# Optimization experiments

Hardware: AMD Instinct MI355X
Metric: run time of the kernel (lower is better)

## Reference

```python
import jax, jax.numpy as jnp
import numpy as np

D = 128

def setup_inputs() -> dict:
    key = jax.random.key(0)
    k1, k2, k3, k4, k5, k6, k7 = jax.random.split(key, 7)
    B, L = 2048, 200
    target = jax.random.normal(k1, (B, D), dtype=jnp.float32)
    item_seq = jax.random.normal(k2, (B, L, D), dtype=jnp.float32)
    seq_len = jax.random.randint(k3, (B,), 0, 200, dtype=jnp.int64 if jax.config.jax_enable_x64 else jnp.int32)
    # MLP params: Linear(4D -> 2D), Linear(2D -> 1), PyTorch-style init scale
    s1 = 1.0 / np.sqrt(4 * D)
    s2 = 1.0 / np.sqrt(2 * D)
    W1 = jax.random.uniform(k4, (4 * D, 2 * D), minval=-s1, maxval=s1, dtype=jnp.float32)
    b1 = jax.random.uniform(k5, (2 * D,), minval=-s1, maxval=s1, dtype=jnp.float32)
    W2 = jax.random.uniform(k6, (2 * D, 1), minval=-s2, maxval=s2, dtype=jnp.float32)
    b2 = jax.random.uniform(k7, (1,), minval=-s2, maxval=s2, dtype=jnp.float32)
    return {"target": target, "item_seq": item_seq, "seq_len": seq_len,
            "W1": W1, "b1": b1, "W2": W2, "b2": b2}

def reference(target, item_seq, seq_len, W1, b1, W2, b2):
    B, L, Dd = item_seq.shape
    t = target[:, None, :]                              # B 1 D (broadcast over L)
    tgt = jnp.broadcast_to(t, (B, L, Dd))
    sub = item_seq - tgt
    dot = item_seq * tgt
    mlp_in = jnp.concatenate([tgt, item_seq, sub, dot], axis=-1)   # B L 4D
    h = jax.nn.relu(jnp.einsum('blf,fh->blh', mlp_in, W1) + b1)    # B L 2D
    score = jnp.einsum('blh,ho->blo', h, W2) + b2                  # B L 1
    mask = (jnp.arange(L)[None, :] < seq_len[:, None]).astype(item_seq.dtype)  # B L
    weighted = score * item_seq * mask[:, :, None]                 # B L D
    return jnp.sum(weighted, axis=1)                               # B D
```

## Files before the change

### kernel.cpp

```cpp
#include <hip/hip_runtime.h>
#include <hip/hip_bf16.h>

typedef short short8 __attribute__((ext_vector_type(8)));
typedef float f32x4 __attribute__((ext_vector_type(4)));

#define XSTRIDE 264

static __device__ inline short f2bf(float f) {
    unsigned u = __float_as_uint(f);
    unsigned r = (u + 0x7fffu + ((u >> 16) & 1u)) >> 16;
    return (short)r;
}
static __device__ inline float bf2f(short s) {
    return __uint_as_float(((unsigned)(unsigned short)s) << 16);
}

__global__ void prep(const float* __restrict__ W1, float* __restrict__ Wu,
                     short* __restrict__ Wfrag, float* __restrict__ out) {
    int idx = blockIdx.x * 256 + threadIdx.x;
    if (idx < 32768) {
        Wu[idx] = W1[idx] - W1[idx + 256 * 256];
    } else if (idx < 98304) {
        int i = idx - 32768;
        int j = i & 7;
        int l = (i >> 3) & 63;
        int s = (i >> 9) & 7;
        int t = i >> 12;
        int k = s * 32 + ((l >> 4) << 3) + j;
        int n = t * 16 + (l & 15);
        float v;
        if (k < 128) v = W1[(128 + k) * 256 + n] + W1[(256 + k) * 256 + n];
        else         v = W1[(384 + (k - 128)) * 256 + n];
        Wfrag[i] = f2bf(v);
    } else {
        out[idx - 98304] = 0.f;
    }
}

__launch_bounds__(256, 2)
__global__ void din_main(const float* __restrict__ target, const float* __restrict__ item_seq,
                         const int* __restrict__ seq_len, const float* __restrict__ W2,
                         const float* __restrict__ b2p, const short* __restrict__ Wfrag,
                         const float* __restrict__ Wu, const float* __restrict__ b1,
                         float* __restrict__ out) {
    const int bid = blockIdx.x;
    const int b = bid >> 1;
    const int half = bid & 1;
    const int tid = threadIdx.x;
    const int lane = tid & 63;
    const int wave = tid >> 6;
    const int col = lane & 15;
    const int q = lane >> 4;

    const int slen = seq_len[b];
    const int nt = (slen + 15) >> 4;
    const int h0 = (nt + 1) >> 1;
    const int t0 = half ? h0 : 0;
    const int t1 = half ? nt : h0;
    if (t0 >= t1) return;

    __shared__ __attribute__((aligned(16))) short Xl[16 * XSTRIDE];
    __shared__ __attribute__((aligned(16))) float tshared[128];
    __shared__ float u_s[256];
    __shared__ float w2_s[256];
    __shared__ float scoreP[4][16];
    __shared__ float out_s[128];

    const float b2 = b2p[0];

    const int r = tid >> 4;
    const int c = (tid & 15) << 3;

    float4 v0, v1;
    {
        int lr = t0 * 16 + r;
        if (lr > 199) lr = 199;
        const float4* src = (const float4*)(item_seq + (((size_t)b * 200 + lr) * 128 + c));
        v0 = src[0]; v1 = src[1];
    }

    if (tid < 128) tshared[tid] = target[b * 128 + tid];
    w2_s[tid] = W2[tid];
    __syncthreads();

    {
        float uacc = b1[tid];
#pragma unroll 8
        for (int d = 0; d < 128; ++d) uacc += tshared[d] * Wu[d * 256 + tid];
        u_s[tid] = uacc;
    }

    float tgt8[8];
    {
        const float4* t4 = (const float4*)(tshared + c);
        float4 ta = t4[0], tb = t4[1];
        tgt8[0] = ta.x; tgt8[1] = ta.y; tgt8[2] = ta.z; tgt8[3] = ta.w;
        tgt8[4] = tb.x; tgt8[5] = tb.y; tgt8[6] = tb.z; tgt8[7] = tb.w;
    }

    short8 bfrag[4][8];
    {
        const short* base = Wfrag + ((size_t)(wave * 32) * 64 + lane) * 8;
#pragma unroll
        for (int i = 0; i < 4; i++)
#pragma unroll
            for (int s = 0; s < 8; s++)
                bfrag[i][s] = *(const short8*)(base + (size_t)((i * 8 + s) * 64) * 8);
    }

    float out_val = 0.f;
    f32x4 acc[4];

    for (int mt = t0; mt < t1; ++mt) {
        const int l0 = mt * 16;
        __syncthreads();

        {
            float v[8] = {v0.x, v0.y, v0.z, v0.w, v1.x, v1.y, v1.z, v1.w};
            short8 p0, p1;
#pragma unroll
            for (int i = 0; i < 8; i++) {
                p0[i] = f2bf(v[i]);
                p1[i] = f2bf(v[i] * tgt8[i]);
            }
            short* xr = Xl + r * XSTRIDE;
            *(short8*)(xr + c) = p0;
            *(short8*)(xr + 128 + c) = p1;
        }
        __syncthreads();

        if (mt + 1 < t1) {
            int lr = l0 + 16 + r;
            if (lr > 199) lr = 199;
            const float4* src = (const float4*)(item_seq + (((size_t)b * 200 + lr) * 128 + c));
            v0 = src[0]; v1 = src[1];
        }

#pragma unroll
        for (int i = 0; i < 4; i++) acc[i] = (f32x4){0.f, 0.f, 0.f, 0.f};

        const short* arow = Xl + col * XSTRIDE + q * 8;
#pragma unroll
        for (int s = 0; s < 8; s++) {
            short8 afrag = *(const short8*)(arow + s * 32);
#pragma unroll
            for (int i = 0; i < 4; i++)
                acc[i] = __builtin_amdgcn_mfma_f32_16x16x32_bf16(afrag, bfrag[i][s], acc[i], 0, 0, 0);
        }

        float sv[4] = {0.f, 0.f, 0.f, 0.f};
#pragma unroll
        for (int i = 0; i < 4; i++) {
            int j = (wave * 4 + i) * 16 + col;
            float uj = u_s[j], wj = w2_s[j];
#pragma unroll
            for (int rg = 0; rg < 4; rg++) {
                float h = acc[i][rg] + uj;
                h = h > 0.f ? h : 0.f;
                sv[rg] += h * wj;
            }
        }
#pragma unroll
        for (int off = 1; off < 16; off <<= 1) {
#pragma unroll
            for (int rg = 0; rg < 4; rg++) sv[rg] += __shfl_xor(sv[rg], off, 64);
        }
        if (col == 0) {
#pragma unroll
            for (int rg = 0; rg < 4; rg++) scoreP[wave][q * 4 + rg] = sv[rg];
        }
        __syncthreads();

        {
            int d = tid & 127;
            int mbase = (tid >> 7) * 8;
#pragma unroll
            for (int mm = 0; mm < 8; mm++) {
                int m = mbase + mm;
                int l = l0 + m;
                float s = scoreP[0][m] + scoreP[1][m] + scoreP[2][m] + scoreP[3][m] + b2;
                s = (l < slen) ? s : 0.f;
                out_val += s * bf2f(Xl[m * XSTRIDE + d]);
            }
        }
    }

    __syncthreads();
    if (tid >= 128) out_s[tid - 128] = out_val;
    __syncthreads();
    if (tid < 128) atomicAdd(&out[b * 128 + tid], out_val + out_s[tid]);
}

extern "C" void kernel_launch(void* const* d_in, const int* in_sizes, int n_in,
                              void* d_out, int out_size, void* d_ws, size_t ws_size,
                              hipStream_t stream) {
    const float* target   = (const float*)d_in[0];
    const float* item_seq = (const float*)d_in[1];
    const int*   seq_len  = (const int*)d_in[2];
    const float* W1       = (const float*)d_in[3];
    const float* b1       = (const float*)d_in[4];
    const float* W2       = (const float*)d_in[5];
    const float* b2       = (const float*)d_in[6];
    float* out = (float*)d_out;

    char* ws = (char*)d_ws;
    float* Wu    = (float*)ws;
    short* Wfrag = (short*)(ws + 131072);

    prep<<<1408, 256, 0, stream>>>(W1, Wu, Wfrag, out);
    din_main<<<4096, 256, 0, stream>>>(target, item_seq, seq_len, W2, b2, Wfrag, Wu, b1, out);
}
```

Before: 349.8 us.

## Hoist per-batch bias GEMV to separate kernel, widen main block to 8 waves with double buffering

Moves the per-row target·(W1a−W1c)+b1 projection out of the main kernel into a batched compute_u kernel that processes 8 rows per block, so each main block no longer runs a 128-step serial GEMV. The main kernel now uses 512 threads (8 waves), each wave holding 2 instead of 4 B-fragment column tiles, which cuts register pressure and raises the launch-bounds occupancy target. The X tile in LDS is double-buffered, which removes one barrier per iteration. The trade-offs are an extra kernel launch, a U buffer round-trip through global memory, and more cross-wave reduction work.

```diff
diff --git a/kernel.cpp b/kernel.cpp
--- a/kernel.cpp
+++ b/kernel.cpp
@@ -15,13 +15,11 @@
     return __uint_as_float(((unsigned)(unsigned short)s) << 16);
 }
 
-__global__ void prep(const float* __restrict__ W1, float* __restrict__ Wu,
-                     short* __restrict__ Wfrag, float* __restrict__ out) {
+__global__ void prep(const float* __restrict__ W1, short* __restrict__ Wfrag,
+                     float* __restrict__ out) {
     int idx = blockIdx.x * 256 + threadIdx.x;
-    if (idx < 32768) {
-        Wu[idx] = W1[idx] - W1[idx + 256 * 256];
-    } else if (idx < 98304) {
-        int i = idx - 32768;
+    if (idx < 65536) {
+        int i = idx;
         int j = i & 7;
         int l = (i >> 3) & 63;
         int s = (i >> 9) & 7;
@@ -33,16 +31,35 @@
         else         v = W1[(384 + (k - 128)) * 256 + n];
         Wfrag[i] = f2bf(v);
     } else {
-        out[idx - 98304] = 0.f;
-    }
-}
-
-__launch_bounds__(256, 2)
+        out[idx - 65536] = 0.f;
+    }
+}
+
+__global__ void compute_u(const float* __restrict__ target, const float* __restrict__ W1,
+                          const float* __restrict__ b1, float* __restrict__ U) {
+    const int b8 = blockIdx.x;
+    const int tid = threadIdx.x;
+    __shared__ float tl[1024];
+#pragma unroll
+    for (int k = 0; k < 4; k++) tl[k * 256 + tid] = target[b8 * 1024 + k * 256 + tid];
+    __syncthreads();
+    float acc[8] = {0.f, 0.f, 0.f, 0.f, 0.f, 0.f, 0.f, 0.f};
+#pragma unroll 8
+    for (int d = 0; d < 128; ++d) {
+        float wud = W1[d * 256 + tid] - W1[(256 + d) * 256 + tid];
+#pragma unroll
+        for (int r = 0; r < 8; r++) acc[r] += tl[r * 128 + d] * wud;
+    }
+    float bj = b1[tid];
+#pragma unroll
+    for (int r = 0; r < 8; r++) U[(b8 * 8 + r) * 256 + tid] = acc[r] + bj;
+}
+
+__launch_bounds__(512, 4)
 __global__ void din_main(const float* __restrict__ target, const float* __restrict__ item_seq,
                          const int* __restrict__ seq_len, const float* __restrict__ W2,
                          const float* __restrict__ b2p, const short* __restrict__ Wfrag,
-                         const float* __restrict__ Wu, const float* __restrict__ b1,
-                         float* __restrict__ out) {
+                         const float* __restrict__ U, float* __restrict__ out) {
     const int bid = blockIdx.x;
     const int b = bid >> 1;
     const int half = bid & 1;
@@ -59,106 +76,94 @@
     const int t1 = half ? nt : h0;
     if (t0 >= t1) return;
 
-    __shared__ __attribute__((aligned(16))) short Xl[16 * XSTRIDE];
-    __shared__ __attribute__((aligned(16))) float tshared[128];
-    __shared__ float u_s[256];
-    __shared__ float w2_s[256];
-    __shared__ float scoreP[4][16];
-    __shared__ float out_s[128];
+    __shared__ __attribute__((aligned(16))) short Xl[2][16 * XSTRIDE];
+    __shared__ __attribute__((aligned(16))) float scoreP[16][8];
+    __shared__ float out_s[3][128];
 
     const float b2 = b2p[0];
 
-    const int r = tid >> 4;
-    const int c = (tid & 15) << 3;
+    const int r = tid >> 5;
+    const int c8 = (tid & 31) << 3;
+    const int cl = c8 & 127;
+    const bool dotpart = (c8 >= 128);
+
+    float tgt8[8];
+    {
+        const float4* t4 = (const float4*)(target + b * 128 + cl);
+        float4 ta = t4[0], tb = t4[1];
+        tgt8[0] = ta.x; tgt8[1] = ta.y; tgt8[2] = ta.z; tgt8[3] = ta.w;
+        tgt8[4] = tb.x; tgt8[5] = tb.y; tgt8[6] = tb.z; tgt8[7] = tb.w;
+    }
+
+    const int j0 = (wave * 2 + 0) * 16 + col;
+    const int j1 = (wave * 2 + 1) * 16 + col;
+    const float u0 = U[b * 256 + j0], u1 = U[b * 256 + j1];
+    const float w20 = W2[j0], w21 = W2[j1];
+
+    short8 bfrag[2][8];
+    {
+        const short* base = Wfrag + ((size_t)(wave * 16) * 64 + lane) * 8;
+#pragma unroll
+        for (int i = 0; i < 2; i++)
+#pragma unroll
+            for (int s = 0; s < 8; s++)
+                bfrag[i][s] = *(const short8*)(base + (size_t)((i * 8 + s) * 64) * 8);
+    }
 
     float4 v0, v1;
     {
         int lr = t0 * 16 + r;
         if (lr > 199) lr = 199;
-        const float4* src = (const float4*)(item_seq + (((size_t)b * 200 + lr) * 128 + c));
+        const float4* src = (const float4*)(item_seq + (((size_t)b * 200 + lr) * 128 + cl));
         v0 = src[0]; v1 = src[1];
     }
 
-    if (tid < 128) tshared[tid] = target[b * 128 + tid];
-    w2_s[tid] = W2[tid];
-    __syncthreads();
-
-    {
-        float uacc = b1[tid];
-#pragma unroll 8
-        for (int d = 0; d < 128; ++d) uacc += tshared[d] * Wu[d * 256 + tid];
-        u_s[tid] = uacc;
-    }
-
-    float tgt8[8];
-    {
-        const float4* t4 = (const float4*)(tshared + c);
-        float4 ta = t4[0], tb = t4[1];
-        tgt8[0] = ta.x; tgt8[1] = ta.y; tgt8[2] = ta.z; tgt8[3] = ta.w;
-        tgt8[4] = tb.x; tgt8[5] = tb.y; tgt8[6] = tb.z; tgt8[7] = tb.w;
-    }
-
-    short8 bfrag[4][8];
-    {
-        const short* base = Wfrag + ((size_t)(wave * 32) * 64 + lane) * 8;
-#pragma unroll
-        for (int i = 0; i < 4; i++)
-#pragma unroll
-            for (int s = 0; s < 8; s++)
-                bfrag[i][s] = *(const short8*)(base + (size_t)((i * 8 + s) * 64) * 8);
-    }
-
+    const int d = tid & 127;
+    const int g = tid >> 7;
     float out_val = 0.f;
-    f32x4 acc[4];
+    f32x4 acc[2];
 
     for (int mt = t0; mt < t1; ++mt) {
         const int l0 = mt * 16;
-        __syncthreads();
+        short* xb = Xl[mt & 1];
 
         {
             float v[8] = {v0.x, v0.y, v0.z, v0.w, v1.x, v1.y, v1.z, v1.w};
-            short8 p0, p1;
-#pragma unroll
-            for (int i = 0; i < 8; i++) {
-                p0[i] = f2bf(v[i]);
-                p1[i] = f2bf(v[i] * tgt8[i]);
+            short8 p;
+            if (dotpart) {
+#pragma unroll
+                for (int i = 0; i < 8; i++) p[i] = f2bf(v[i] * tgt8[i]);
+            } else {
+#pragma unroll
+                for (int i = 0; i < 8; i++) p[i] = f2bf(v[i]);
             }
-            short* xr = Xl + r * XSTRIDE;
-            *(short8*)(xr + c) = p0;
-            *(short8*)(xr + 128 + c) = p1;
+            *(short8*)(xb + r * XSTRIDE + c8) = p;
         }
         __syncthreads();
 
         if (mt + 1 < t1) {
             int lr = l0 + 16 + r;
             if (lr > 199) lr = 199;
-            const float4* src = (const float4*)(item_seq + (((size_t)b * 200 + lr) * 128 + c));
+            const float4* src = (const float4*)(item_seq + (((size_t)b * 200 + lr) * 128 + cl));
             v0 = src[0]; v1 = src[1];
         }
 
-#pragma unroll
-        for (int i = 0; i < 4; i++) acc[i] = (f32x4){0.f, 0.f, 0.f, 0.f};
-
-        const short* arow = Xl + col * XSTRIDE + q * 8;
+        acc[0] = (f32x4){0.f, 0.f, 0.f, 0.f};
+        acc[1] = (f32x4){0.f, 0.f, 0.f, 0.f};
+        const short* arow = xb + col * XSTRIDE + q * 8;
 #pragma unroll
         for (int s = 0; s < 8; s++) {
             short8 afrag = *(const short8*)(arow + s * 32);
-#pragma unroll
-            for (int i = 0; i < 4; i++)
-                acc[i] = __builtin_amdgcn_mfma_f32_16x16x32_bf16(afrag, bfrag[i][s], acc[i], 0, 0, 0);
-        }
-
-        float sv[4] = {0.f, 0.f, 0.f, 0.f};
-#pragma unroll
-        for (int i = 0; i < 4; i++) {
-            int j = (wave * 4 + i) * 16 + col;
-            float uj = u_s[j], wj = w2_s[j];
-#pragma unroll
-            for (int rg = 0; rg < 4; rg++) {
-                float h = acc[i][rg] + uj;
-                h = h > 0.f ? h : 0.f;
-                sv[rg] += h * wj;
-            }
+            acc[0] = __builtin_amdgcn_mfma_f32_16x16x32_bf16(afrag, bfrag[0][s], acc[0], 0, 0, 0);
+            acc[1] = __builtin_amdgcn_mfma_f32_16x16x32_bf16(afrag, bfrag[1][s], acc[1], 0, 0, 0);
+        }
+
+        float sv[4];
+#pragma unroll
+        for (int rg = 0; rg < 4; rg++) {
+            float ha = acc[0][rg] + u0; ha = ha > 0.f ? ha : 0.f;
+            float hb = acc[1][rg] + u1; hb = hb > 0.f ? hb : 0.f;
+            sv[rg] = ha * w20 + hb * w21;
         }
 #pragma unroll
         for (int off = 1; off < 16; off <<= 1) {
@@ -167,28 +172,26 @@
         }
         if (col == 0) {
 #pragma unroll
-            for (int rg = 0; rg < 4; rg++) scoreP[wave][q * 4 + rg] = sv[rg];
+            for (int rg = 0; rg < 4; rg++) scoreP[q * 4 + rg][wave] = sv[rg];
         }
         __syncthreads();
 
-        {
-            int d = tid & 127;
-            int mbase = (tid >> 7) * 8;
-#pragma unroll
-            for (int mm = 0; mm < 8; mm++) {
-                int m = mbase + mm;
-                int l = l0 + m;
-                float s = scoreP[0][m] + scoreP[1][m] + scoreP[2][m] + scoreP[3][m] + b2;
-                s = (l < slen) ? s : 0.f;
-                out_val += s * bf2f(Xl[m * XSTRIDE + d]);
-            }
+#pragma unroll
+        for (int mm = 0; mm < 4; mm++) {
+            int m = g * 4 + mm;
+            int l = l0 + m;
+            const float4* sp = (const float4*)&scoreP[m][0];
+            float4 s0 = sp[0], s1 = sp[1];
+            float s = ((s0.x + s0.y) + (s0.z + s0.w)) + ((s1.x + s1.y) + (s1.z + s1.w)) + b2;
+            s = (l < slen) ? s : 0.f;
+            out_val += s * bf2f(xb[m * XSTRIDE + d]);
         }
     }
 
     __syncthreads();
-    if (tid >= 128) out_s[tid - 128] = out_val;
+    if (g > 0) out_s[g - 1][d] = out_val;
     __syncthreads();
-    if (tid < 128) atomicAdd(&out[b * 128 + tid], out_val + out_s[tid]);
+    if (g == 0) atomicAdd(&out[b * 128 + d], out_val + out_s[0][d] + out_s[1][d] + out_s[2][d]);
 }
 
 extern "C" void kernel_launch(void* const* d_in, const int* in_sizes, int n_in,
@@ -204,9 +207,10 @@
     float* out = (float*)d_out;
 
     char* ws = (char*)d_ws;
-    float* Wu    = (float*)ws;
-    short* Wfrag = (short*)(ws + 131072);
-
-    prep<<<1408, 256, 0, stream>>>(W1, Wu, Wfrag, out);
-    din_main<<<4096, 256, 0, stream>>>(target, item_seq, seq_len, W2, b2, Wfrag, Wu, b1, out);
-}
+    short* Wfrag = (short*)ws;
+    float* U     = (float*)(ws + 131072);
+
+    prep<<<1280, 256, 0, stream>>>(W1, Wfrag, out);
+    compute_u<<<256, 256, 0, stream>>>(target, W1, b1, U);
+    din_main<<<4096, 512, 0, stream>>>(target, item_seq, seq_len, W2, b2, Wfrag, U, out);
+}
```

Result: faster. 339.9 us (-2.8%).
